# Kernel optimization log

Measured on AMD Instinct MI355X. Metric: run time of the kernel, lower is better.

Reference implementation:

```python
import jax, jax.numpy as jnp
import numpy as np

N_JOINTS = 16
N_VERTS = 778
# standard MANO kinematic tree (parent of joint i; root parent is -1, unused)
PARENTS = np.array([-1, 0, 1, 2, 0, 4, 5, 0, 7, 8, 0, 10, 11, 0, 13, 14])
# rotate_base=True: root rotation is post-multiplied by 180-deg rotation about x
ROT_X = np.array([[1.0, 0.0, 0.0], [0.0, -1.0, 0.0], [0.0, 0.0, -1.0]], dtype=np.float32)


def _batch_rodrigues(theta):
    # theta: [M, 3] axis-angle -> [M, 3, 3] rotation matrices (via quaternion, HMR-style)
    angle = jnp.linalg.norm(theta + 1e-8, axis=1, keepdims=True)
    axis = theta / angle
    half = 0.5 * angle
    quat = jnp.concatenate([jnp.cos(half), jnp.sin(half) * axis], axis=1)
    quat = quat / jnp.linalg.norm(quat, axis=1, keepdims=True)
    w, x, y, z = quat[:, 0], quat[:, 1], quat[:, 2], quat[:, 3]
    w2, x2, y2, z2 = w * w, x * x, y * y, z * z
    wx, wy, wz = w * x, w * y, w * z
    xy, xz, yz = x * y, x * z, y * z
    R = jnp.stack([
        w2 + x2 - y2 - z2, 2 * xy - 2 * wz, 2 * wy + 2 * xz,
        2 * wz + 2 * xy, w2 - x2 + y2 - z2, 2 * yz - 2 * wx,
        2 * xz - 2 * wy, 2 * wx + 2 * yz, w2 - x2 - y2 + z2,
    ], axis=1)
    return R.reshape(-1, 3, 3)


def _make_A(R, t):
    # R: [N,3,3], t: [N,3] -> [N,4,4] homogeneous transform
    top = jnp.concatenate([R, t[:, :, None]], axis=2)          # [N,3,4]
    bot = jnp.broadcast_to(jnp.array([0.0, 0.0, 0.0, 1.0], R.dtype), (R.shape[0], 1, 4))
    return jnp.concatenate([top, bot], axis=1)


def _global_rigid_transform(Rs, J):
    # Rs: [N,16,3,3], J: [N,16,3]
    root_rotation = jnp.matmul(Rs[:, 0], jnp.asarray(ROT_X, Rs.dtype))
    results = [_make_A(root_rotation, J[:, 0])]
    for i in range(1, N_JOINTS):
        p = int(PARENTS[i])
        t = J[:, i] - J[:, p]
        results.append(jnp.matmul(results[p], _make_A(Rs[:, i], t)))
    G = jnp.stack(results, axis=1)                              # [N,16,4,4]
    J_transformed = G[:, :, :3, 3]
    # A = G - pad(G[:, :, :3, :3] @ J) : remove joint-rest translation
    rel = jnp.einsum('njab,njb->nja', G[:, :, :3, :3], J)       # [N,16,3]
    A = G.at[:, :, :3, 3].add(-rel)
    return J_transformed, A


def setup_inputs() -> dict:
    key = jax.random.key(0)
    ks = jax.random.split(key, 7)
    N = 4096
    return {
        'beta': jax.random.normal(ks[0], (N, 10), jnp.float32),
        'theta': jax.random.normal(ks[1], (N, 48), jnp.float32) * 0.3,
        'v_template': jax.random.normal(ks[2], (N_VERTS, 3), jnp.float32) * 0.1,
        'shapedirs': jax.random.normal(ks[3], (10, N_VERTS * 3), jnp.float32) * 0.01,
        'J_regressor': jax.random.uniform(ks[4], (N_VERTS, N_JOINTS), jnp.float32) / N_VERTS,
        'posedirs': jax.random.normal(ks[5], (135, N_VERTS * 3), jnp.float32) * 0.01,
        'weights': jax.random.uniform(ks[6], (N_VERTS, N_JOINTS), jnp.float32),
    }


def reference(beta, theta, v_template, shapedirs, J_regressor, posedirs, weights):
    N = beta.shape[0]
    # shape blendshapes
    v_shaped = jnp.matmul(beta, shapedirs).reshape(N, N_VERTS, 3) + v_template
    # rest joints from vertices
    J = jnp.einsum('nvc,vj->njc', v_shaped, J_regressor)        # [N,16,3]
    # pose rotations
    Rs = _batch_rodrigues(theta.reshape(-1, 3)).reshape(N, N_JOINTS, 3, 3)
    # pose blendshapes (exclude root)
    pose_feature = (Rs[:, 1:] - jnp.eye(3, dtype=Rs.dtype)).reshape(N, 135)
    v_posed = jnp.matmul(pose_feature, posedirs).reshape(N, N_VERTS, 3) + v_shaped
    # kinematic chain
    J_transformed, A = _global_rigid_transform(Rs, J)
    # linear blend skinning
    T = jnp.einsum('vj,njab->nvab', weights, A)                 # [N,778,4,4]
    ones = jnp.ones((N, N_VERTS, 1), v_posed.dtype)
    v_homo = jnp.concatenate([v_posed, ones], axis=2)           # [N,778,4]
    verts = jnp.einsum('nvab,nvb->nva', T, v_homo)[:, :, :3]    # [N,778,3]
    joints = jnp.einsum('nvc,vj->njc', verts, J_regressor)      # [N,16,3]
    return verts, joints, Rs
```

## Files before the change

### kernel.cpp

```cpp
#include <hip/hip_runtime.h>
#include <math.h>

#define NJ 16
#define NV 778
#define M3 2334
#define NTB 156

typedef float f32x4  __attribute__((ext_vector_type(4)));
typedef short bf16x8 __attribute__((ext_vector_type(8)));

__device__ __forceinline__ unsigned short f2bf(float x) {
    unsigned int u = __float_as_uint(x);
    unsigned int r = (u + 0x7FFF + ((u >> 16) & 1)) >> 16;
    return (unsigned short)r;
}

__device__ __forceinline__ void rodrigues9(
    float t0, float t1, float t2,
    float& r0, float& r1, float& r2, float& r3, float& r4,
    float& r5, float& r6, float& r7, float& r8)
{
    const float eps = 1e-8f;
    float a0 = t0 + eps, a1 = t1 + eps, a2 = t2 + eps;
    float angle = sqrtf(a0*a0 + a1*a1 + a2*a2);
    float inv  = 1.0f / angle;
    float half = 0.5f * angle;
    float sh = sinf(half), chh = cosf(half);
    float qw = chh;
    float qx = sh * t0 * inv;
    float qy = sh * t1 * inv;
    float qz = sh * t2 * inv;
    float qn = 1.0f / sqrtf(qw*qw + qx*qx + qy*qy + qz*qz);
    qw *= qn; qx *= qn; qy *= qn; qz *= qn;
    float w2=qw*qw, x2=qx*qx, y2=qy*qy, z2=qz*qz;
    float wx=qw*qx, wy=qw*qy, wz=qw*qz;
    float xy=qx*qy, xz=qx*qz, yz=qy*qz;
    r0 = w2 + x2 - y2 - z2;
    r1 = 2.f*(xy - wz);
    r2 = 2.f*(wy + xz);
    r3 = 2.f*(wz + xy);
    r4 = w2 - x2 + y2 - z2;
    r5 = 2.f*(yz - wx);
    r6 = 2.f*(xz - wy);
    r7 = 2.f*(wx + yz);
    r8 = w2 - x2 - y2 + z2;
}


__global__ __launch_bounds__(256, 1) void k01_prep(
    const float* __restrict__ shapedirs,
    const float* __restrict__ posedirs,
    const float* __restrict__ Jreg,
    const float* __restrict__ vtemp,
    const float* __restrict__ theta,
    const float* __restrict__ beta,
    float* __restrict__ SJJT,
    float* __restrict__ RsOut,
    bf16x8* __restrict__ Bf,
    bf16x8* __restrict__ Af,
    int N)
{
    const int tid = threadIdx.x;
    const int rodBlocks = (N * NJ) / 256;
    const int nB = NTB * 5 * 64;
    const int bfBlocks = nB / 256;
    if (blockIdx.x < 44) {
        int task = blockIdx.x * 4 + (tid >> 6);
        int lane = tid & 63;
        if (task < 176) {
            int b = task >> 4;
            int j = task & 15;
            const float* src = (b < 10) ? (shapedirs + (size_t)b * M3) : vtemp;
            float a0 = 0.f, a1 = 0.f, a2 = 0.f;
            for (int v = lane; v < NV; v += 64) {
                float jr = Jreg[v * 16 + j];
                a0 = fmaf(src[v*3 + 0], jr, a0);
                a1 = fmaf(src[v*3 + 1], jr, a1);
                a2 = fmaf(src[v*3 + 2], jr, a2);
            }
#pragma unroll
            for (int m = 1; m < 64; m <<= 1) {
                a0 += __shfl_xor(a0, m);
                a1 += __shfl_xor(a1, m);
                a2 += __shfl_xor(a2, m);
            }
            if (lane == 0) {
                int base = (b < 10) ? (b*48 + j*3) : (480 + j*3);
                SJJT[base + 0] = a0;
                SJJT[base + 1] = a1;
                SJJT[base + 2] = a2;
            }
        }
        return;
    }
    if (blockIdx.x < 44 + rodBlocks) {
        int idx = (blockIdx.x - 44) * 256 + tid;
        int n = idx >> 4;
        int j = idx & 15;
        float r0,r1,r2,r3,r4,r5,r6,r7,r8;
        rodrigues9(theta[n*48 + j*3 + 0], theta[n*48 + j*3 + 1],
                   theta[n*48 + j*3 + 2], r0,r1,r2,r3,r4,r5,r6,r7,r8);
        float* R = RsOut + (size_t)idx * 9;
        R[0]=r0; R[1]=r1; R[2]=r2; R[3]=r3; R[4]=r4;
        R[5]=r5; R[6]=r6; R[7]=r7; R[8]=r8;
        return;
    }
    if (blockIdx.x < 44 + rodBlocks + bfBlocks) {
        int idx = (blockIdx.x - 44 - rodBlocks) * 256 + tid;
        int lane = idx & 63;
        int ks   = (idx >> 6) % 5;
        int nt   = idx / 320;
        int col = nt * 16 + (lane & 15);
        int k0  = ks * 32 + (lane >> 4) * 8;
        bf16x8 o;
#pragma unroll
        for (int j = 0; j < 8; ++j) {
            int k = k0 + j;
            float val = 0.f;
            if (col < M3) {
                if (k < 10)       val = shapedirs[(size_t)k * M3 + col];
                else if (k < 145) val = posedirs[(size_t)(k - 10) * M3 + col];
            }
            o[j] = (short)f2bf(val);
        }
        Bf[idx] = o;
        return;
    }
    int idx = (blockIdx.x - 44 - rodBlocks - bfBlocks) * 256 + tid;
    int nA = (N / 16) * 5 * 64;
    if (idx >= nA) return;
    int lane = idx & 63;
    int ks   = (idx >> 6) % 5;
    int mt   = idx / 320;
    int n  = mt * 16 + (lane & 15);
    int k0 = ks * 32 + (lane >> 4) * 8;

    int kkA = k0 - 10;
    int jA  = (kkA < 0) ? 0 : (kkA > 134 ? 14 : kkA / 9);
    int kkB = k0 - 3;
    int jB  = (kkB < 0) ? 0 : (kkB > 134 ? 14 : kkB / 9);

    float ra0,ra1,ra2,ra3,ra4,ra5,ra6,ra7,ra8;
    rodrigues9(theta[n*48 + (jA+1)*3 + 0], theta[n*48 + (jA+1)*3 + 1],
               theta[n*48 + (jA+1)*3 + 2], ra0,ra1,ra2,ra3,ra4,ra5,ra6,ra7,ra8);
    float rb0,rb1,rb2,rb3,rb4,rb5,rb6,rb7,rb8;
    rodrigues9(theta[n*48 + (jB+1)*3 + 0], theta[n*48 + (jB+1)*3 + 1],
               theta[n*48 + (jB+1)*3 + 2], rb0,rb1,rb2,rb3,rb4,rb5,rb6,rb7,rb8);

    bf16x8 o;
#pragma unroll
    for (int j = 0; j < 8; ++j) {
        int k = k0 + j;
        float val;
        if (k < 10) {
            val = beta[(size_t)n * 10 + k];
        } else if (k < 145) {
            int kk = k - 10;
            int jj = kk / 9;
            int rr = kk - jj * 9;
            float sa = (rr==0)?ra0:(rr==1)?ra1:(rr==2)?ra2:(rr==3)?ra3:
                       (rr==4)?ra4:(rr==5)?ra5:(rr==6)?ra6:(rr==7)?ra7:ra8;
            float sb = (rr==0)?rb0:(rr==1)?rb1:(rr==2)?rb2:(rr==3)?rb3:
                       (rr==4)?rb4:(rr==5)?rb5:(rr==6)?rb6:(rr==7)?rb7:rb8;
            float vv = (jj == jA) ? sa : sb;
            if ((rr & 3) == 0) vv -= 1.f;
            val = vv;
        } else {
            val = 0.f;
        }
        o[j] = (short)f2bf(val);
    }
    Af[idx] = o;
}

__global__ __launch_bounds__(256, 1) void k2c_chain(
    const float* __restrict__ beta,
    const float* __restrict__ Rs,
    const float* __restrict__ SJJT,
    float* __restrict__ Aws,
    float* __restrict__ joints,
    int N)
{
    const int tid = threadIdx.x;
    const int KB = (N * 5 + 255) / 256;
    if (blockIdx.x >= KB) {
        int idx = (blockIdx.x - KB) * 256 + tid;
        if (idx < N * 48) joints[idx] = 0.f;
        return;
    }
    __shared__ float sS[528];
    for (int i = tid; i < 528; i += 256) sS[i] = SJJT[i];
    __syncthreads();
    int gid = blockIdx.x * 256 + tid;
    if (gid >= N * 5) return;
    int n  = gid / 5;
    int ch = gid % 5;

    float b[10];
#pragma unroll
    for (int i = 0; i < 10; ++i) b[i] = beta[n*10 + i];

    int jidx[4];
    jidx[0] = 0; jidx[1] = ch*3 + 1; jidx[2] = ch*3 + 2; jidx[3] = ch*3 + 3;
    float J[4][3];
#pragma unroll
    for (int q = 0; q < 4; ++q) {
        int j = jidx[q];
#pragma unroll
        for (int c = 0; c < 3; ++c) {
            float acc = sS[480 + j*3 + c];
#pragma unroll
            for (int qq = 0; qq < 10; ++qq)
                acc = fmaf(b[qq], sS[qq*48 + j*3 + c], acc);
            J[q][c] = acc;
        }
    }

    const float* Rn = Rs + (size_t)n * 144;
    float* An = Aws + (size_t)n * 192;

    float GpR[9], Gpt[3];
#pragma unroll
    for (int r = 0; r < 3; ++r) {
        GpR[r*3+0] =  Rn[r*3+0];
        GpR[r*3+1] = -Rn[r*3+1];
        GpR[r*3+2] = -Rn[r*3+2];
    }
    Gpt[0] = J[0][0]; Gpt[1] = J[0][1]; Gpt[2] = J[0][2];

    if (ch == 0) {
#pragma unroll
        for (int r = 0; r < 3; ++r) {
            float rel = GpR[r*3+0]*J[0][0] + GpR[r*3+1]*J[0][1] + GpR[r*3+2]*J[0][2];
            An[r*4 + 0] = GpR[r*3+0];
            An[r*4 + 1] = GpR[r*3+1];
            An[r*4 + 2] = GpR[r*3+2];
            An[r*4 + 3] = Gpt[r] - rel;
        }
    }

#pragma unroll
    for (int st = 0; st < 3; ++st) {
        int i = jidx[st+1];
        const float* Ri = Rn + (size_t)i * 9;
        float t0 = J[st+1][0] - J[st][0];
        float t1 = J[st+1][1] - J[st][1];
        float t2 = J[st+1][2] - J[st][2];
        float GR[9], Gt[3];
#pragma unroll
        for (int r = 0; r < 3; ++r) {
#pragma unroll
            for (int c = 0; c < 3; ++c)
                GR[r*3+c] = GpR[r*3+0]*Ri[c] + GpR[r*3+1]*Ri[3+c] + GpR[r*3+2]*Ri[6+c];
            Gt[r] = GpR[r*3+0]*t0 + GpR[r*3+1]*t1 + GpR[r*3+2]*t2 + Gpt[r];
        }
#pragma unroll
        for (int r = 0; r < 3; ++r) {
            float rel = GR[r*3+0]*J[st+1][0] + GR[r*3+1]*J[st+1][1] + GR[r*3+2]*J[st+1][2];
            An[i*12 + r*4 + 0] = GR[r*3+0];
            An[i*12 + r*4 + 1] = GR[r*3+1];
            An[i*12 + r*4 + 2] = GR[r*3+2];
            An[i*12 + r*4 + 3] = Gt[r] - rel;
        }
#pragma unroll
        for (int r = 0; r < 9; ++r) GpR[r] = GR[r];
        Gpt[0] = Gt[0]; Gpt[1] = Gt[1]; Gpt[2] = Gt[2];
    }
}

__global__ __launch_bounds__(256, 1) void k34_gemm_blend(
    const bf16x8* __restrict__ Af,
    const bf16x8* __restrict__ Bf,
    const float* __restrict__ vtemp,
    const float* __restrict__ Aws,
    const float* __restrict__ weights,
    const float* __restrict__ Jreg,
    float* __restrict__ verts,
    float* __restrict__ joints,
    int N)
{
    __shared__ float sC[16][194];
    const int tid  = threadIdx.x;
    const int w    = tid >> 6;
    const int lane = tid & 63;
    const int mt   = blockIdx.x;
    const int ntb  = blockIdx.y * 12 + w * 3;

    f32x4 acc0 = {0.f,0.f,0.f,0.f};
    f32x4 acc1 = {0.f,0.f,0.f,0.f};
    f32x4 acc2 = {0.f,0.f,0.f,0.f};

    const bf16x8* Ab = Af + (size_t)mt * 5 * 64 + lane;
    const bf16x8* Bb = Bf + lane;

#pragma unroll
    for (int ks = 0; ks < 5; ++ks) {
        bf16x8 a  = Ab[ks * 64];
        bf16x8 b0 = Bb[((size_t)(ntb+0) * 5 + ks) * 64];
        bf16x8 b1 = Bb[((size_t)(ntb+1) * 5 + ks) * 64];
        bf16x8 b2 = Bb[((size_t)(ntb+2) * 5 + ks) * 64];
        acc0 = __builtin_amdgcn_mfma_f32_16x16x32_bf16(a, b0, acc0, 0, 0, 0);
        acc1 = __builtin_amdgcn_mfma_f32_16x16x32_bf16(a, b1, acc1, 0, 0, 0);
        acc2 = __builtin_amdgcn_mfma_f32_16x16x32_bf16(a, b2, acc2, 0, 0, 0);
    }

    {
        const int rl = (lane >> 4) * 4;
        const int cl = w * 48 + (lane & 15);
#pragma unroll
        for (int r = 0; r < 4; ++r) {
            sC[rl + r][cl +  0] = acc0[r];
            sC[rl + r][cl + 16] = acc1[r];
            sC[rl + r][cl + 32] = acc2[r];
        }
    }
    __syncthreads();

    const int vg = blockIdx.y * 64 + lane;
    const bool valid = vg < NV;
    const int cvg = valid ? vg : (NV - 1);

    const float4* wrow = reinterpret_cast<const float4*>(&weights[(size_t)cvg * 16]);
    float vtx = vtemp[cvg*3 + 0];
    float vty = vtemp[cvg*3 + 1];
    float vtz = vtemp[cvg*3 + 2];

    float res[12];
#pragma unroll
    for (int it = 0; it < 4; ++it) {
        const int nl = w * 4 + it;
        const int n  = __builtin_amdgcn_readfirstlane(mt * 16 + nl);
        const float* An = Aws + (size_t)n * 192;

        float px = sC[nl][lane*3 + 0] + vtx;
        float py = sC[nl][lane*3 + 1] + vty;
        float pz = sC[nl][lane*3 + 2] + vtz;

        float ox = 0.f, oy = 0.f, oz = 0.f;
#pragma unroll
        for (int q = 0; q < 4; ++q) {
            float4 wq = wrow[q];
#define BJQ(jj_, ww_) { \
            const float* ap = An + (4*q + jj_) * 12; \
            float a0=ap[0], a1=ap[1], a2 =ap[2],  a3 =ap[3]; \
            float a4=ap[4], a5=ap[5], a6 =ap[6],  a7 =ap[7]; \
            float a8=ap[8], a9=ap[9], a10=ap[10], a11=ap[11]; \
            float X = fmaf(a0,px, fmaf(a1,py, fmaf(a2,pz, a3))); \
            float Y = fmaf(a4,px, fmaf(a5,py, fmaf(a6,pz, a7))); \
            float Z = fmaf(a8,px, fmaf(a9,py, fmaf(a10,pz, a11))); \
            ox = fmaf(ww_, X, ox); oy = fmaf(ww_, Y, oy); oz = fmaf(ww_, Z, oz); }
            BJQ(0, wq.x) BJQ(1, wq.y) BJQ(2, wq.z) BJQ(3, wq.w)
#undef BJQ
        }
        res[it*3+0] = ox; res[it*3+1] = oy; res[it*3+2] = oz;
    }
    __syncthreads();

#pragma unroll
    for (int it = 0; it < 4; ++it) {
        const int nl = w * 4 + it;
        sC[nl][lane*3 + 0] = res[it*3+0];
        sC[nl][lane*3 + 1] = res[it*3+1];
        sC[nl][lane*3 + 2] = res[it*3+2];
        if (valid) {
            float* o = verts + (size_t)(mt*16 + nl) * M3 + (size_t)vg * 3;
            o[0] = res[it*3+0]; o[1] = res[it*3+1]; o[2] = res[it*3+2];
        }
    }
    __syncthreads();

    {
        const int s  = tid >> 4;
        const int j  = tid & 15;
        const int vb = blockIdx.y * 64;
        float a0 = 0.f, a1 = 0.f, a2 = 0.f;
#pragma unroll 4
        for (int v = 0; v < 64; ++v) {
            float jr = (vb + v < NV) ? Jreg[(size_t)(vb + v) * 16 + j] : 0.f;
            a0 = fmaf(jr, sC[s][v*3 + 0], a0);
            a1 = fmaf(jr, sC[s][v*3 + 1], a1);
            a2 = fmaf(jr, sC[s][v*3 + 2], a2);
        }
        float* jp = joints + (size_t)(mt * 16 + s) * 48 + j * 3;
        atomicAdd(&jp[0], a0);
        atomicAdd(&jp[1], a1);
        atomicAdd(&jp[2], a2);
    }
}

extern "C" void kernel_launch(void* const* d_in, const int* in_sizes, int n_in,
                              void* d_out, int out_size, void* d_ws, size_t ws_size,
                              hipStream_t stream)
{
    const float* beta   = (const float*)d_in[0];
    const float* theta  = (const float*)d_in[1];
    const float* vtemp  = (const float*)d_in[2];
    const float* shaped = (const float*)d_in[3];
    const float* Jreg   = (const float*)d_in[4];
    const float* posed  = (const float*)d_in[5];
    const float* wts    = (const float*)d_in[6];
    float* out = (float*)d_out;
    const int N = in_sizes[0] / 10;

    float* verts  = out;
    float* joints = out + (size_t)N * M3;
    float* RsOut  = joints + (size_t)N * 48;
    float* Aws    = (float*)d_ws;
    float*  fbase = Aws + (size_t)N * 192;
    const int nA = (N / 16) * 5 * 64;
    const int nB = NTB * 5 * 64;
    bf16x8* Af    = (bf16x8*)fbase;
    bf16x8* Bf    = (bf16x8*)(fbase + (size_t)nA * 4);
    float*  sjjt  = fbase + (size_t)nA * 4 + (size_t)nB * 4;

    const int rodBlocks = (N * NJ) / 256;
    const int zeroBlocks = (N * 48 + 255) / 256;

    k01_prep<<<44 + rodBlocks + nB/256 + nA/256, 256, 0, stream>>>(
        shaped, posed, Jreg, vtemp, theta, beta, sjjt, RsOut, Bf, Af, N);
    k2c_chain<<<(N*5 + 255)/256 + zeroBlocks, 256, 0, stream>>>(
        beta, RsOut, sjjt, Aws, joints, N);
    k34_gemm_blend<<<dim3(N/16, 13), 256, 0, stream>>>(
        Af, Bf, vtemp, Aws, wts, Jreg, verts, joints, N);
}
```

Baseline: 69.77 us.

## Double vertex tile per block to 128 vertices, halving joint atomics and A reloads

Each block of the fused GEMM+blend kernel now covers 128 vertices instead of 64. Each wave computes six MFMA tiles and each lane skins two vertices. This reuses the per-sample transform matrices across twice the vertices and halves the grid's y dimension, cutting joint atomicAdd traffic and repeated loads of A and weights. In exchange it raises register pressure, uses more shared memory, and pads B to 168 tiles, which adds wasted work on the tail block.

```diff
diff --git a/kernel.cpp b/kernel.cpp
--- a/kernel.cpp
+++ b/kernel.cpp
@@ -4,7 +4,7 @@
 #define NJ 16
 #define NV 778
 #define M3 2334
-#define NTB 156
+#define NTB 168
 
 typedef float f32x4  __attribute__((ext_vector_type(4)));
 typedef short bf16x8 __attribute__((ext_vector_type(8)));
@@ -279,16 +279,20 @@
     float* __restrict__ joints,
     int N)
 {
-    __shared__ float sC[16][194];
+    __shared__ __attribute__((aligned(16))) float sC[16 * 386];
+#define SCg(r_, c_) sC[(r_) * 386 + (c_)]
     const int tid  = threadIdx.x;
     const int w    = tid >> 6;
     const int lane = tid & 63;
     const int mt   = blockIdx.x;
-    const int ntb  = blockIdx.y * 12 + w * 3;
+    const int ntb0 = blockIdx.y * 24 + w * 6;
 
     f32x4 acc0 = {0.f,0.f,0.f,0.f};
     f32x4 acc1 = {0.f,0.f,0.f,0.f};
     f32x4 acc2 = {0.f,0.f,0.f,0.f};
+    f32x4 acc3 = {0.f,0.f,0.f,0.f};
+    f32x4 acc4 = {0.f,0.f,0.f,0.f};
+    f32x4 acc5 = {0.f,0.f,0.f,0.f};
 
     const bf16x8* Ab = Af + (size_t)mt * 5 * 64 + lane;
     const bf16x8* Bb = Bf + lane;
@@ -296,75 +300,104 @@
 #pragma unroll
     for (int ks = 0; ks < 5; ++ks) {
         bf16x8 a  = Ab[ks * 64];
-        bf16x8 b0 = Bb[((size_t)(ntb+0) * 5 + ks) * 64];
-        bf16x8 b1 = Bb[((size_t)(ntb+1) * 5 + ks) * 64];
-        bf16x8 b2 = Bb[((size_t)(ntb+2) * 5 + ks) * 64];
+        bf16x8 b0 = Bb[((size_t)(ntb0+0) * 5 + ks) * 64];
+        bf16x8 b1 = Bb[((size_t)(ntb0+1) * 5 + ks) * 64];
+        bf16x8 b2 = Bb[((size_t)(ntb0+2) * 5 + ks) * 64];
+        bf16x8 b3 = Bb[((size_t)(ntb0+3) * 5 + ks) * 64];
+        bf16x8 b4 = Bb[((size_t)(ntb0+4) * 5 + ks) * 64];
+        bf16x8 b5 = Bb[((size_t)(ntb0+5) * 5 + ks) * 64];
         acc0 = __builtin_amdgcn_mfma_f32_16x16x32_bf16(a, b0, acc0, 0, 0, 0);
         acc1 = __builtin_amdgcn_mfma_f32_16x16x32_bf16(a, b1, acc1, 0, 0, 0);
         acc2 = __builtin_amdgcn_mfma_f32_16x16x32_bf16(a, b2, acc2, 0, 0, 0);
+        acc3 = __builtin_amdgcn_mfma_f32_16x16x32_bf16(a, b3, acc3, 0, 0, 0);
+        acc4 = __builtin_amdgcn_mfma_f32_16x16x32_bf16(a, b4, acc4, 0, 0, 0);
+        acc5 = __builtin_amdgcn_mfma_f32_16x16x32_bf16(a, b5, acc5, 0, 0, 0);
     }
 
     {
         const int rl = (lane >> 4) * 4;
-        const int cl = w * 48 + (lane & 15);
+        const int cl = w * 96 + (lane & 15);
 #pragma unroll
         for (int r = 0; r < 4; ++r) {
-            sC[rl + r][cl +  0] = acc0[r];
-            sC[rl + r][cl + 16] = acc1[r];
-            sC[rl + r][cl + 32] = acc2[r];
+            SCg(rl + r, cl +  0) = acc0[r];
+            SCg(rl + r, cl + 16) = acc1[r];
+            SCg(rl + r, cl + 32) = acc2[r];
+            SCg(rl + r, cl + 48) = acc3[r];
+            SCg(rl + r, cl + 64) = acc4[r];
+            SCg(rl + r, cl + 80) = acc5[r];
         }
     }
     __syncthreads();
 
-    const int vg = blockIdx.y * 64 + lane;
-    const bool valid = vg < NV;
-    const int cvg = valid ? vg : (NV - 1);
-
-    const float4* wrow = reinterpret_cast<const float4*>(&weights[(size_t)cvg * 16]);
-    float vtx = vtemp[cvg*3 + 0];
-    float vty = vtemp[cvg*3 + 1];
-    float vtz = vtemp[cvg*3 + 2];
-
-    float res[12];
+    const int vgA = blockIdx.y * 128 + lane;
+    const int vgB = vgA + 64;
+    const bool valA = vgA < NV;
+    const bool valB = vgB < NV;
+    const int cvA = valA ? vgA : (NV - 1);
+    const int cvB = valB ? vgB : (NV - 1);
+
+    const float4* wrA = reinterpret_cast<const float4*>(&weights[(size_t)cvA * 16]);
+    const float4* wrB = reinterpret_cast<const float4*>(&weights[(size_t)cvB * 16]);
+    float vtxA = vtemp[cvA*3+0], vtyA = vtemp[cvA*3+1], vtzA = vtemp[cvA*3+2];
+    float vtxB = vtemp[cvB*3+0], vtyB = vtemp[cvB*3+1], vtzB = vtemp[cvB*3+2];
+
+    float res[24];
 #pragma unroll
     for (int it = 0; it < 4; ++it) {
         const int nl = w * 4 + it;
         const int n  = __builtin_amdgcn_readfirstlane(mt * 16 + nl);
         const float* An = Aws + (size_t)n * 192;
 
-        float px = sC[nl][lane*3 + 0] + vtx;
-        float py = sC[nl][lane*3 + 1] + vty;
-        float pz = sC[nl][lane*3 + 2] + vtz;
-
-        float ox = 0.f, oy = 0.f, oz = 0.f;
+        float pxA = SCg(nl, lane*3 + 0) + vtxA;
+        float pyA = SCg(nl, lane*3 + 1) + vtyA;
+        float pzA = SCg(nl, lane*3 + 2) + vtzA;
+        float pxB = SCg(nl, 192 + lane*3 + 0) + vtxB;
+        float pyB = SCg(nl, 192 + lane*3 + 1) + vtyB;
+        float pzB = SCg(nl, 192 + lane*3 + 2) + vtzB;
+
+        float oxA=0.f, oyA=0.f, ozA=0.f, oxB=0.f, oyB=0.f, ozB=0.f;
 #pragma unroll
         for (int q = 0; q < 4; ++q) {
-            float4 wq = wrow[q];
-#define BJQ(jj_, ww_) { \
+            float4 wqA = wrA[q];
+            float4 wqB = wrB[q];
+#define BJQ2(jj_, wwA_, wwB_) { \
             const float* ap = An + (4*q + jj_) * 12; \
             float a0=ap[0], a1=ap[1], a2 =ap[2],  a3 =ap[3]; \
             float a4=ap[4], a5=ap[5], a6 =ap[6],  a7 =ap[7]; \
             float a8=ap[8], a9=ap[9], a10=ap[10], a11=ap[11]; \
-            float X = fmaf(a0,px, fmaf(a1,py, fmaf(a2,pz, a3))); \
-            float Y = fmaf(a4,px, fmaf(a5,py, fmaf(a6,pz, a7))); \
-            float Z = fmaf(a8,px, fmaf(a9,py, fmaf(a10,pz, a11))); \
-            ox = fmaf(ww_, X, ox); oy = fmaf(ww_, Y, oy); oz = fmaf(ww_, Z, oz); }
-            BJQ(0, wq.x) BJQ(1, wq.y) BJQ(2, wq.z) BJQ(3, wq.w)
-#undef BJQ
-        }
-        res[it*3+0] = ox; res[it*3+1] = oy; res[it*3+2] = oz;
+            float X = fmaf(a0,pxA, fmaf(a1,pyA, fmaf(a2,pzA, a3))); \
+            float Y = fmaf(a4,pxA, fmaf(a5,pyA, fmaf(a6,pzA, a7))); \
+            float Z = fmaf(a8,pxA, fmaf(a9,pyA, fmaf(a10,pzA, a11))); \
+            oxA = fmaf(wwA_, X, oxA); oyA = fmaf(wwA_, Y, oyA); ozA = fmaf(wwA_, Z, ozA); \
+            X = fmaf(a0,pxB, fmaf(a1,pyB, fmaf(a2,pzB, a3))); \
+            Y = fmaf(a4,pxB, fmaf(a5,pyB, fmaf(a6,pzB, a7))); \
+            Z = fmaf(a8,pxB, fmaf(a9,pyB, fmaf(a10,pzB, a11))); \
+            oxB = fmaf(wwB_, X, oxB); oyB = fmaf(wwB_, Y, oyB); ozB = fmaf(wwB_, Z, ozB); }
+            BJQ2(0, wqA.x, wqB.x) BJQ2(1, wqA.y, wqB.y)
+            BJQ2(2, wqA.z, wqB.z) BJQ2(3, wqA.w, wqB.w)
+#undef BJQ2
+        }
+        res[it*6+0] = oxA; res[it*6+1] = oyA; res[it*6+2] = ozA;
+        res[it*6+3] = oxB; res[it*6+4] = oyB; res[it*6+5] = ozB;
     }
     __syncthreads();
 
 #pragma unroll
     for (int it = 0; it < 4; ++it) {
         const int nl = w * 4 + it;
-        sC[nl][lane*3 + 0] = res[it*3+0];
-        sC[nl][lane*3 + 1] = res[it*3+1];
-        sC[nl][lane*3 + 2] = res[it*3+2];
-        if (valid) {
-            float* o = verts + (size_t)(mt*16 + nl) * M3 + (size_t)vg * 3;
-            o[0] = res[it*3+0]; o[1] = res[it*3+1]; o[2] = res[it*3+2];
+        SCg(nl, lane*3 + 0)       = valA ? res[it*6+0] : 0.f;
+        SCg(nl, lane*3 + 1)       = valA ? res[it*6+1] : 0.f;
+        SCg(nl, lane*3 + 2)       = valA ? res[it*6+2] : 0.f;
+        SCg(nl, 192 + lane*3 + 0) = valB ? res[it*6+3] : 0.f;
+        SCg(nl, 192 + lane*3 + 1) = valB ? res[it*6+4] : 0.f;
+        SCg(nl, 192 + lane*3 + 2) = valB ? res[it*6+5] : 0.f;
+        if (valA) {
+            float* o = verts + (size_t)(mt*16 + nl) * M3 + (size_t)vgA * 3;
+            o[0] = res[it*6+0]; o[1] = res[it*6+1]; o[2] = res[it*6+2];
+        }
+        if (valB) {
+            float* o = verts + (size_t)(mt*16 + nl) * M3 + (size_t)vgB * 3;
+            o[0] = res[it*6+3]; o[1] = res[it*6+4]; o[2] = res[it*6+5];
         }
     }
     __syncthreads();
@@ -372,20 +405,21 @@
     {
         const int s  = tid >> 4;
         const int j  = tid & 15;
-        const int vb = blockIdx.y * 64;
+        const int vb = blockIdx.y * 128;
         float a0 = 0.f, a1 = 0.f, a2 = 0.f;
 #pragma unroll 4
-        for (int v = 0; v < 64; ++v) {
+        for (int v = 0; v < 128; ++v) {
             float jr = (vb + v < NV) ? Jreg[(size_t)(vb + v) * 16 + j] : 0.f;
-            a0 = fmaf(jr, sC[s][v*3 + 0], a0);
-            a1 = fmaf(jr, sC[s][v*3 + 1], a1);
-            a2 = fmaf(jr, sC[s][v*3 + 2], a2);
+            a0 = fmaf(jr, SCg(s, v*3 + 0), a0);
+            a1 = fmaf(jr, SCg(s, v*3 + 1), a1);
+            a2 = fmaf(jr, SCg(s, v*3 + 2), a2);
         }
         float* jp = joints + (size_t)(mt * 16 + s) * 48 + j * 3;
         atomicAdd(&jp[0], a0);
         atomicAdd(&jp[1], a1);
         atomicAdd(&jp[2], a2);
     }
+#undef SCg
 }
 
 extern "C" void kernel_launch(void* const* d_in, const int* in_sizes, int n_in,
@@ -420,6 +454,6 @@
         shaped, posed, Jreg, vtemp, theta, beta, sjjt, RsOut, Bf, Af, N);
     k2c_chain<<<(N*5 + 255)/256 + zeroBlocks, 256, 0, stream>>>(
         beta, RsOut, sjjt, Aws, joints, N);
-    k34_gemm_blend<<<dim3(N/16, 13), 256, 0, stream>>>(
+    k34_gemm_blend<<<dim3(N/16, 7), 256, 0, stream>>>(
         Af, Bf, vtemp, Aws, wts, Jreg, verts, joints, N);
 }
```

Measured after the change: 85.64 us. +22.7%, slower.
